# Optimization experiments

Measured on AMD Instinct MI355X. Metric: run time of the kernel, lower is better.

Reference implementation:

```python
import jax, jax.numpy as jnp
import numpy as np

NEG_SLOPE = 0.1

def setup_inputs() -> dict:
    key = jax.random.key(0)
    k1, k2, k3 = jax.random.split(key, 3)
    b, d = 256, 1024
    cf = jax.random.normal(k1, (b, d), dtype=jnp.float32)
    pf = jax.random.normal(k2, (b, d), dtype=jnp.float32)
    # nn.Linear(d*d, 1): weight (1, d*d), bias (1,); kaiming-uniform-ish scale
    lim = 1.0 / np.sqrt(d * d)
    W = jax.random.uniform(k3, (1, d * d), dtype=jnp.float32, minval=-lim, maxval=lim)
    bias = jnp.zeros((1,), dtype=jnp.float32)
    return {"cf": cf, "pf": pf, "W": W, "bias": bias}

def reference(cf, pf, W, bias):
    b, d = cf.shape
    # outer product: (b, d, d) -> flatten (b, d*d)
    outer = jnp.einsum('bi,bj->bij', cf, pf).reshape(b, d * d)
    x = jnp.where(outer >= 0, outer, NEG_SLOPE * outer)  # LeakyReLU(0.1)
    return x @ W.T + bias  # (b, 1)
```

## Files before the change

kernel.cpp:

```cpp
#include <hip/hip_runtime.h>
#include <hip/hip_bf16.h>
#include <math.h>


constexpr int B = 256, D = 1024;
constexpr int BN = 32;
constexpr int JC = 64;
constexpr int NT = D / BN;
constexpr int KC = D / JC;
constexpr int NBLK = NT * KC;
constexpr int LDP = 72;

typedef __attribute__((ext_vector_type(8))) short bf16x8;
typedef __attribute__((ext_vector_type(4))) short bf16x4;
typedef __attribute__((ext_vector_type(4))) float f32x4;
typedef __attribute__((ext_vector_type(4))) int   int32x4;

__device__ __forceinline__ ushort f2bf(float x) {
    __hip_bfloat16 h = __float2bfloat16(x);
    return *reinterpret_cast<ushort*>(&h);
}

__device__ __forceinline__ bf16x8 cvt8(float4 lo, float4 hi) {
    bf16x8 v;
    v[0] = (short)f2bf(lo.x); v[1] = (short)f2bf(lo.y);
    v[2] = (short)f2bf(lo.z); v[3] = (short)f2bf(lo.w);
    v[4] = (short)f2bf(hi.x); v[5] = (short)f2bf(hi.y);
    v[6] = (short)f2bf(hi.z); v[7] = (short)f2bf(hi.w);
    return v;
}

__global__ __launch_bounds__(512) void opl_main(
    const float* __restrict__ cf, const float* __restrict__ pf,
    const float* __restrict__ W, float* __restrict__ ws)
{
    __shared__ ushort sP[B][LDP];
    __shared__ ushort sW[BN][LDP];

    const int nt = blockIdx.x & (NT - 1);
    const int kc = blockIdx.x >> 5;
    const int ibase = nt * BN, jbase = kc * JC;
    const int t = threadIdx.x;

    {
        const int r = t >> 4, c = (t & 15) * 4;
        const float4 v = *reinterpret_cast<const float4*>(&W[(size_t)(ibase + r) * D + jbase + c]);
        bf16x4 o;
        o[0] = (short)f2bf(v.x); o[1] = (short)f2bf(v.y);
        o[2] = (short)f2bf(v.z); o[3] = (short)f2bf(v.w);
        *reinterpret_cast<bf16x4*>(&sW[r][c]) = o;
    }
    #pragma unroll
    for (int p = 0; p < 4; ++p) {
        const int r = p * 64 + (t >> 3), c = (t & 7) * 8;
        const float* src = &pf[(size_t)r * D + jbase + c];
        const float4 lo = *reinterpret_cast<const float4*>(src);
        const float4 hi = *reinterpret_cast<const float4*>(src + 4);
        *reinterpret_cast<bf16x8*>(&sP[r][c]) = cvt8(lo, hi);
    }

    const int lane = t & 63;
    const int wid = t >> 6;
    const int mwave = wid * 32;
    const int r16 = lane & 15;
    const int g = lane >> 4;

    float cfv[2][2][4];
    #pragma unroll
    for (int mf = 0; mf < 2; ++mf)
        #pragma unroll
        for (int nf = 0; nf < 2; ++nf)
            #pragma unroll
            for (int r = 0; r < 4; ++r)
                cfv[mf][nf][r] = cf[(size_t)(mwave + mf * 16 + g * 4 + r) * D + ibase + nf * 16 + r16];

    __syncthreads();

    f32x4 accG[2][2] = {};
    f32x4 accH[2][2] = {};

    #pragma unroll
    for (int ks = 0; ks < JC / 32; ++ks) {
        const int c0 = ks * 32 + g * 8;
        bf16x8 a[2], b[2];
        #pragma unroll
        for (int mf = 0; mf < 2; ++mf)
            a[mf] = *reinterpret_cast<const bf16x8*>(&sP[mwave + mf * 16 + r16][c0]);
        #pragma unroll
        for (int nf = 0; nf < 2; ++nf)
            b[nf] = *reinterpret_cast<const bf16x8*>(&sW[nf * 16 + r16][c0]);
        #pragma unroll
        for (int mf = 0; mf < 2; ++mf) {
            int32x4 ai = __builtin_bit_cast(int32x4, a[mf]);
            ai &= 0x7fff7fff;
            const bf16x8 aa = __builtin_bit_cast(bf16x8, ai);
            #pragma unroll
            for (int nf = 0; nf < 2; ++nf) {
                accG[mf][nf] = __builtin_amdgcn_mfma_f32_16x16x32_bf16(a[mf], b[nf], accG[mf][nf], 0, 0, 0);
                accH[mf][nf] = __builtin_amdgcn_mfma_f32_16x16x32_bf16(aa,    b[nf], accH[mf][nf], 0, 0, 0);
            }
        }
    }

    float s[2][4];
    #pragma unroll
    for (int mf = 0; mf < 2; ++mf)
        #pragma unroll
        for (int r = 0; r < 4; ++r) s[mf][r] = 0.f;

    #pragma unroll
    for (int mf = 0; mf < 2; ++mf) {
        #pragma unroll
        for (int nf = 0; nf < 2; ++nf) {
            #pragma unroll
            for (int r = 0; r < 4; ++r) {
                const float c = cfv[mf][nf][r];
                s[mf][r] = fmaf(0.55f * c, accG[mf][nf][r],
                           fmaf(0.45f * fabsf(c), accH[mf][nf][r], s[mf][r]));
            }
        }
    }
    #pragma unroll
    for (int mf = 0; mf < 2; ++mf) {
        #pragma unroll
        for (int r = 0; r < 4; ++r) {
            float v = s[mf][r];
            v += __shfl_xor(v, 1);
            v += __shfl_xor(v, 2);
            v += __shfl_xor(v, 4);
            v += __shfl_xor(v, 8);
            s[mf][r] = v;
        }
    }
    if (r16 == 0) {
        #pragma unroll
        for (int mf = 0; mf < 2; ++mf)
            #pragma unroll
            for (int r = 0; r < 4; ++r)
                ws[(size_t)(mwave + mf * 16 + g * 4 + r) * NBLK + blockIdx.x] = s[mf][r];
    }
}

__global__ __launch_bounds__(256) void opl_reduce(
    const float* __restrict__ ws, const float* __restrict__ bias,
    float* __restrict__ out)
{
    const int wid = threadIdx.x >> 6, lane = threadIdx.x & 63;
    const int b = blockIdx.x * 4 + wid;
    const float* p = ws + (size_t)b * NBLK;
    float s = 0.f;
    #pragma unroll
    for (int k = 0; k < NBLK / 64; ++k) s += p[lane + k * 64];
    #pragma unroll
    for (int off = 1; off < 64; off <<= 1) s += __shfl_xor(s, off);
    if (lane == 0) out[b] = s + bias[0];
}

extern "C" void kernel_launch(void* const* d_in, const int* in_sizes, int n_in,
                              void* d_out, int out_size, void* d_ws, size_t ws_size,
                              hipStream_t stream) {
    const float* cf   = (const float*)d_in[0];
    const float* pf   = (const float*)d_in[1];
    const float* W    = (const float*)d_in[2];
    const float* bias = (const float*)d_in[3];
    float* out = (float*)d_out;
    float* ws  = (float*)d_ws;

    opl_main<<<NT * KC, 512, 0, stream>>>(cf, pf, W, ws);
    opl_reduce<<<B / 4, 256, 0, stream>>>(ws, bias, out);
}
```

Measured before the change: 12.77 us.

## Fuse cross-block reduction into main kernel via atomic counters

```diff
diff --git a/kernel.cpp b/kernel.cpp
--- a/kernel.cpp
+++ b/kernel.cpp
@@ -9,6 +9,7 @@
 constexpr int NT = D / BN;
 constexpr int KC = D / JC;
 constexpr int NBLK = NT * KC;
+constexpr int GRP = 16, NGRP = NBLK / GRP;
 constexpr int LDP = 72;
 
 typedef __attribute__((ext_vector_type(8))) short bf16x8;
@@ -30,12 +31,23 @@
     return v;
 }
 
-__global__ __launch_bounds__(512) void opl_main(
+constexpr size_t PART_F = (size_t)NBLK * B;
+constexpr size_t WS2_F  = (size_t)NGRP * B;
+constexpr size_t CNT_OFF_F = PART_F + WS2_F;
+constexpr size_t WS_NEED = (CNT_OFF_F + NGRP + 1) * 4;
+
+__global__ __launch_bounds__(512) void opl_fused(
     const float* __restrict__ cf, const float* __restrict__ pf,
-    const float* __restrict__ W, float* __restrict__ ws)
+    const float* __restrict__ W, float* __restrict__ ws,
+    const float* __restrict__ bias, float* __restrict__ out)
 {
     __shared__ ushort sP[B][LDP];
     __shared__ ushort sW[BN][LDP];
+    __shared__ int sflag;
+
+    float* part = ws;
+    float* ws2  = ws + PART_F;
+    int*   cnt  = (int*)(ws + CNT_OFF_F);
 
     const int nt = blockIdx.x & (NT - 1);
     const int kc = blockIdx.x >> 5;
@@ -133,27 +145,123 @@
         }
     }
     if (r16 == 0) {
-        #pragma unroll
-        for (int mf = 0; mf < 2; ++mf)
-            #pragma unroll
-            for (int r = 0; r < 4; ++r)
-                ws[(size_t)(mwave + mf * 16 + g * 4 + r) * NBLK + blockIdx.x] = s[mf][r];
-    }
-}
-
-__global__ __launch_bounds__(256) void opl_reduce(
-    const float* __restrict__ ws, const float* __restrict__ bias,
-    float* __restrict__ out)
+        float* dst = part + (size_t)blockIdx.x * B;
+        #pragma unroll
+        for (int mf = 0; mf < 2; ++mf) {
+            f32x4 v = {s[mf][0], s[mf][1], s[mf][2], s[mf][3]};
+            *reinterpret_cast<f32x4*>(&dst[mwave + mf * 16 + g * 4]) = v;
+        }
+    }
+
+    const int grp = blockIdx.x >> 4;
+    __syncthreads();
+    if (t == 0) {
+        __threadfence();
+        sflag = (atomicAdd(&cnt[grp], 1) == GRP - 1) ? 1 : 0;
+    }
+    __syncthreads();
+    if (sflag) {
+        __threadfence();
+        if (t < B) {
+            float acc = 0.f;
+            #pragma unroll
+            for (int k = 0; k < GRP; ++k)
+                acc += part[(size_t)(grp * GRP + k) * B + t];
+            ws2[(size_t)grp * B + t] = acc;
+        }
+        __syncthreads();
+        if (t == 0) {
+            __threadfence();
+            sflag = (atomicAdd(&cnt[NGRP], 1) == NGRP - 1) ? 1 : 0;
+        }
+        __syncthreads();
+        if (sflag) {
+            __threadfence();
+            if (t < B) {
+                float acc = 0.f;
+                #pragma unroll
+                for (int g2 = 0; g2 < NGRP; ++g2)
+                    acc += ws2[(size_t)g2 * B + t];
+                out[t] = acc + bias[0];
+            }
+        }
+    }
+}
+
+__global__ __launch_bounds__(256) void opl_init_fb(float* __restrict__ out,
+                                                   const float* __restrict__ bias) {
+    out[threadIdx.x] = bias[0];
+}
+
+__global__ __launch_bounds__(256, 2) void opl_valu_fb(
+    const float* __restrict__ cf, const float* __restrict__ pf,
+    const float* __restrict__ W, float* __restrict__ out)
 {
-    const int wid = threadIdx.x >> 6, lane = threadIdx.x & 63;
-    const int b = blockIdx.x * 4 + wid;
-    const float* p = ws + (size_t)b * NBLK;
-    float s = 0.f;
-    #pragma unroll
-    for (int k = 0; k < NBLK / 64; ++k) s += p[lane + k * 64];
-    #pragma unroll
-    for (int off = 1; off < 64; off <<= 1) s += __shfl_xor(s, off);
-    if (lane == 0) out[b] = s + bias[0];
+    constexpr int BM = 64, BNf = 64, BK = 32, FKC = 128;
+    const int bid = blockIdx.x;
+    const int mt = bid & 3, ntb = (bid >> 2) & 15, kcb = bid >> 6;
+    const int mbase = mt * BM, nbase = ntb * BNf, kbase = kcb * FKC;
+    __shared__ float sWf[BK][BNf];
+    __shared__ float sC[BK][BM + 4];
+    const int tid = threadIdx.x;
+    const int tx = tid & 15, ty = tid >> 4;
+    const int wr = tid >> 4, wc = (tid & 15) * 4;
+    const int cb = tid >> 3, ci = (tid & 7) * 4;
+    float accG[4][4] = {{0.f}}, accH[4][4] = {{0.f}};
+    for (int k0 = 0; k0 < FKC; k0 += BK) {
+        const int kg = kbase + k0;
+        const float4 w0 = *reinterpret_cast<const float4*>(&W[(size_t)(kg + wr) * D + nbase + wc]);
+        const float4 w1 = *reinterpret_cast<const float4*>(&W[(size_t)(kg + wr + 16) * D + nbase + wc]);
+        const float4 c0 = *reinterpret_cast<const float4*>(&cf[(size_t)(mbase + cb) * D + kg + ci]);
+        const float4 c1 = *reinterpret_cast<const float4*>(&cf[(size_t)(mbase + cb + 32) * D + kg + ci]);
+        *reinterpret_cast<float4*>(&sWf[wr][wc]) = w0;
+        *reinterpret_cast<float4*>(&sWf[wr + 16][wc]) = w1;
+        sC[ci + 0][cb] = c0.x; sC[ci + 1][cb] = c0.y;
+        sC[ci + 2][cb] = c0.z; sC[ci + 3][cb] = c0.w;
+        sC[ci + 0][cb + 32] = c1.x; sC[ci + 1][cb + 32] = c1.y;
+        sC[ci + 2][cb + 32] = c1.z; sC[ci + 3][cb + 32] = c1.w;
+        __syncthreads();
+        #pragma unroll
+        for (int k = 0; k < BK; ++k) {
+            const float4 wv = *reinterpret_cast<const float4*>(&sWf[k][tx * 4]);
+            const float4 cv = *reinterpret_cast<const float4*>(&sC[k][ty * 4]);
+            const float w[4] = {wv.x, wv.y, wv.z, wv.w};
+            const float c[4] = {cv.x, cv.y, cv.z, cv.w};
+            #pragma unroll
+            for (int r = 0; r < 4; ++r) {
+                const float cc = c[r], aa = fabsf(cc);
+                #pragma unroll
+                for (int q = 0; q < 4; ++q) {
+                    accG[r][q] = fmaf(cc, w[q], accG[r][q]);
+                    accH[r][q] = fmaf(aa, w[q], accH[r][q]);
+                }
+            }
+        }
+        __syncthreads();
+    }
+    float sr[4];
+    #pragma unroll
+    for (int r = 0; r < 4; ++r) {
+        const float4 pv = *reinterpret_cast<const float4*>(&pf[(size_t)(mbase + ty * 4 + r) * D + nbase + tx * 4]);
+        const float p[4] = {pv.x, pv.y, pv.z, pv.w};
+        float acc = 0.f;
+        #pragma unroll
+        for (int q = 0; q < 4; ++q)
+            acc += 0.55f * p[q] * accG[r][q] + 0.45f * fabsf(p[q]) * accH[r][q];
+        sr[r] = acc;
+    }
+    #pragma unroll
+    for (int r = 0; r < 4; ++r) {
+        sr[r] += __shfl_xor(sr[r], 1);
+        sr[r] += __shfl_xor(sr[r], 2);
+        sr[r] += __shfl_xor(sr[r], 4);
+        sr[r] += __shfl_xor(sr[r], 8);
+    }
+    if (tx == 0) {
+        #pragma unroll
+        for (int r = 0; r < 4; ++r)
+            atomicAdd(&out[mbase + ty * 4 + r], sr[r]);
+    }
 }
 
 extern "C" void kernel_launch(void* const* d_in, const int* in_sizes, int n_in,
@@ -166,6 +274,12 @@
     float* out = (float*)d_out;
     float* ws  = (float*)d_ws;
 
-    opl_main<<<NT * KC, 512, 0, stream>>>(cf, pf, W, ws);
-    opl_reduce<<<B / 4, 256, 0, stream>>>(ws, bias, out);
-}
+    if (ws_size >= WS_NEED) {
+        int* cnt = (int*)(ws + CNT_OFF_F);
+        hipMemsetAsync(cnt, 0, (NGRP + 1) * sizeof(int), stream);
+        opl_fused<<<NBLK, 512, 0, stream>>>(cf, pf, W, ws, bias, out);
+    } else {
+        opl_init_fb<<<1, 256, 0, stream>>>(out, bias);
+        opl_valu_fb<<<512, 256, 0, stream>>>(cf, pf, W, out);
+    }
+}
```

Measured after the change: 50.29 us. 3.94x slower.
